# Kernel tuning notes

Hardware: AMD Instinct MI355X
Metric: run time of the kernel (lower is better)

Reference implementation:

```python
import jax, jax.numpy as jnp
import numpy as np

HEADS = 12
DIM_HEAD = 64

def setup_inputs() -> dict:
    key = jax.random.key(0)
    ks = jax.random.split(key, 5)
    B, S, D = 4, 2048, 768
    s = 0.02
    return {
        "x": jax.random.normal(ks[0], (B, S, D), dtype=jnp.float32),
        "Wq": jax.random.normal(ks[1], (D, D), dtype=jnp.float32) * s,
        "Wk": jax.random.normal(ks[2], (D, D), dtype=jnp.float32) * s,
        "Wv": jax.random.normal(ks[3], (D, D), dtype=jnp.float32) * s,
        "Wo": jax.random.normal(ks[4], (D, D), dtype=jnp.float32) * s,
        "bo": jnp.zeros((D,), dtype=jnp.float32),
    }

def reference(x, Wq, Wk, Wv, Wo, bo):
    B, S, D = x.shape
    H, Dh = HEADS, DIM_HEAD
    scale = Dh ** -0.5
    # projections (torch Linear: x @ W^T)
    q = (x @ Wq.T).reshape(B, S, H, Dh).transpose(0, 2, 1, 3) * scale  # [B,H,S,Dh]
    k = (x @ Wk.T).reshape(B, S, H, Dh).transpose(0, 2, 1, 3)
    v = (x @ Wv.T).reshape(B, S, H, Dh).transpose(0, 2, 1, 3)
    sim = jnp.einsum("bhid,bhjd->bhij", q, k)  # [B,H,S,S]
    mask_value = -jnp.finfo(sim.dtype).max
    causal_mask = jnp.triu(jnp.ones((S, S), dtype=bool), k=1)
    sim = jnp.where(causal_mask, mask_value, sim)
    attn = jax.nn.softmax(sim, axis=-1)
    # dropout is identity in eval mode
    out = jnp.einsum("bhij,bhjd->bhid", attn, v)  # [B,H,S,Dh]
    out = out.transpose(0, 2, 1, 3).reshape(B, S, H * Dh)
    return out @ Wo.T + bo
```

## Files before the change

### kernel.cpp

```cpp
#include <hip/hip_runtime.h>
#include <stdint.h>

typedef unsigned short u16;
typedef __bf16 bf16x8 __attribute__((ext_vector_type(8)));
typedef float f32x4 __attribute__((ext_vector_type(4)));
typedef u16 u16x4 __attribute__((ext_vector_type(4)));
typedef u16 u16x8 __attribute__((ext_vector_type(8)));
typedef uint32_t u32x2 __attribute__((ext_vector_type(2)));

#define LDS_CAST(p) (reinterpret_cast<__attribute__((address_space(3))) uint32_t*>(reinterpret_cast<uintptr_t>(p)))
#define GLB_CAST(p) (reinterpret_cast<const __attribute__((address_space(1))) uint32_t*>(reinterpret_cast<uintptr_t>(p)))
#define GLOAD16(g, l) __builtin_amdgcn_global_load_lds(GLB_CAST(g), LDS_CAST(l), 16, 0, 0)
#define AS3U16(p) (reinterpret_cast<__attribute__((address_space(3))) u16*>(reinterpret_cast<uintptr_t>(p)))

__device__ __forceinline__ u16 f2bf(float f) {
    uint32_t u = __builtin_bit_cast(uint32_t, f);
    u += 0x7fffu + ((u >> 16) & 1u);
    return (u16)(u >> 16);
}
__device__ __forceinline__ u16 bfbits(float f) {
    return __builtin_bit_cast(u16, (__bf16)f);
}

__global__ void cast_f32_bf16(const float* __restrict__ in, u16* __restrict__ out, int n4) {
    int i = blockIdx.x * blockDim.x + threadIdx.x;
    if (i >= n4) return;
    float4 f = reinterpret_cast<const float4*>(in)[i];
    u16x4 o;
    o.x = f2bf(f.x); o.y = f2bf(f.y); o.z = f2bf(f.z); o.w = f2bf(f.w);
    reinterpret_cast<u16x4*>(out)[i] = o;
}

__global__ void cast_w4(const float* __restrict__ a, const float* __restrict__ b,
                        const float* __restrict__ c, const float* __restrict__ d,
                        u16* __restrict__ oa, u16* __restrict__ ob,
                        u16* __restrict__ oc, u16* __restrict__ od, int n4) {
    const int z = blockIdx.y;
    const float* in = (z == 0) ? a : (z == 1) ? b : (z == 2) ? c : d;
    u16* out = (z == 0) ? oa : (z == 1) ? ob : (z == 2) ? oc : od;
    int i = blockIdx.x * blockDim.x + threadIdx.x;
    if (i >= n4) return;
    float4 f = reinterpret_cast<const float4*>(in)[i];
    u16x4 o;
    o.x = f2bf(f.x); o.y = f2bf(f.y); o.z = f2bf(f.z); o.w = f2bf(f.w);
    reinterpret_cast<u16x4*>(out)[i] = o;
}

__global__ __launch_bounds__(256) void gemm_qkv(
    const u16* __restrict__ X, const u16* __restrict__ Wq,
    const u16* __restrict__ Wk, const u16* __restrict__ Wv,
    u16* __restrict__ qo, u16* __restrict__ ko, u16* __restrict__ vTo)
{
    __shared__ u16 As[2][128 * 32];
    __shared__ u16 Bs[2][128 * 32];
    const int tid = threadIdx.x;
    const int lane = tid & 63;
    const int w = tid >> 6;
    const int lr = lane & 15, lg = lane >> 4;
    const int wrow = (w >> 1) * 64, wcol = (w & 1) * 64;

    const int lin = blockIdx.x + blockIdx.y * 6 + blockIdx.z * 384;
    const int xcd = lin & 7, idx = lin >> 3;
    const int prow = xcd * 8 + idx / 18;
    const int rem = idx % 18;
    const int bxc = rem % 6, z = rem / 6;
    const int row0 = prow * 128, col0 = bxc * 128;
    const u16* Wt = (z == 0) ? Wq : (z == 1) ? Wk : Wv;

    f32x4 acc[4][4];
#pragma unroll
    for (int m = 0; m < 4; ++m)
#pragma unroll
        for (int n = 0; n < 4; ++n)
#pragma unroll
            for (int j = 0; j < 4; ++j) acc[m][n][j] = 0.f;

#define QSTAGE(KT)                                                                                 \
    {                                                                                              \
        const int buf_ = (KT) & 1;                                                                 \
        _Pragma("unroll")                                                                          \
        for (int it = 0; it < 2; ++it) {                                                           \
            const int c = it * 256 + w * 64 + lane;                                                \
            const int row = c >> 2, c16 = c & 3;                                                   \
            GLOAD16(X  + (size_t)(row0 + row) * 768 + (KT) * 32 + c16 * 8, &As[buf_][(it * 256 + w * 64) * 8]); \
            GLOAD16(Wt + (size_t)(col0 + row) * 768 + (KT) * 32 + c16 * 8, &Bs[buf_][(it * 256 + w * 64) * 8]); \
        }                                                                                          \
    }

#define QSTEP(KT, VN, PF)                                                                          \
    {                                                                                              \
        if (PF) QSTAGE((KT) + 1);                                                                  \
        asm volatile("s_waitcnt vmcnt(" #VN ")" ::: "memory");                                     \
        __builtin_amdgcn_s_barrier();                                                              \
        const int cur_ = (KT) & 1;                                                                 \
        bf16x8 af[4], bfr[4];                                                                      \
        _Pragma("unroll")                                                                          \
        for (int m = 0; m < 4; ++m) af[m] = *(const bf16x8*)&As[cur_][(wrow + m * 16 + lr) * 32 + lg * 8]; \
        _Pragma("unroll")                                                                          \
        for (int n = 0; n < 4; ++n) bfr[n] = *(const bf16x8*)&Bs[cur_][(wcol + n * 16 + lr) * 32 + lg * 8]; \
        asm volatile("s_waitcnt lgkmcnt(0)" ::: "memory");                                         \
        __builtin_amdgcn_sched_barrier(0);                                                         \
        __builtin_amdgcn_s_barrier();                                                              \
        _Pragma("unroll")                                                                          \
        for (int m = 0; m < 4; ++m)                                                                \
            _Pragma("unroll")                                                                      \
            for (int n = 0; n < 4; ++n)                                                            \
                acc[m][n] = __builtin_amdgcn_mfma_f32_16x16x32_bf16(af[m], bfr[n], acc[m][n], 0, 0, 0); \
    }

    QSTAGE(0);
    for (int kt = 0; kt < 23; ++kt) QSTEP(kt, 4, true);
    QSTEP(23, 0, false);
#undef QSTEP
#undef QSTAGE

    if (z == 2) {
#pragma unroll
        for (int n = 0; n < 4; ++n) {
            const int j = col0 + wcol + n * 16 + lr;
            const int h = j >> 6, dh = j & 63;
#pragma unroll
            for (int m = 0; m < 4; ++m) {
                const int i0 = row0 + wrow + m * 16 + lg * 4;
                const int b = i0 >> 11, s0 = i0 & 2047;
                u16x4 pk;
#pragma unroll
                for (int r = 0; r < 4; ++r) pk[r] = bfbits(acc[m][n][r]);
                *(u16x4*)&vTo[(((size_t)b * 12 + h) * 64 + dh) * 2048 + s0] = pk;
            }
        }
    } else {
        u16* outp = (z == 0) ? qo : ko;
        const float scl = (z == 0) ? 0.18033688011112042f : 1.0f;
#pragma unroll
        for (int n = 0; n < 4; ++n) {
            const int j = col0 + wcol + n * 16 + lr;
            const int h = j >> 6, dh = j & 63;
#pragma unroll
            for (int m = 0; m < 4; ++m)
#pragma unroll
                for (int r = 0; r < 4; ++r) {
                    const int i = row0 + wrow + m * 16 + lg * 4 + r;
                    const int b = i >> 11, s = i & 2047;
                    outp[(((size_t)b * 12 + h) * 2048 + s) * 64 + dh] = bfbits(acc[m][n][r] * scl);
                }
        }
    }
}

template<bool DIAG>
__device__ __forceinline__ void attn_step(
    const bf16x8* aq, f32x4* o, float* lrow,
    const u16* __restrict__ Ksb, const u16* __restrict__ Vsb, u16* __restrict__ PT,
    int kvb, int qg0, int lr, int lg)
{
    f32x4 sacc[4];
#pragma unroll
    for (int n = 0; n < 4; ++n)
#pragma unroll
        for (int j = 0; j < 4; ++j) sacc[n][j] = 0.f;
    __builtin_amdgcn_s_setprio(1);
#pragma unroll
    for (int kk = 0; kk < 2; ++kk)
#pragma unroll
        for (int n = 0; n < 4; ++n) {
            const int row = n * 16 + lr;
            const int p = (kk * 4 + lg) ^ (row & 7);
            bf16x8 bk = *(const bf16x8*)&Ksb[row * 64 + p * 8];
            sacc[n] = __builtin_amdgcn_mfma_f32_16x16x32_bf16(aq[kk], bk, sacc[n], 0, 0, 0);
        }
    __builtin_amdgcn_s_setprio(0);

    float pv[4][4];
#pragma unroll
    for (int r = 0; r < 4; ++r) {
        float ls = 0.f;
#pragma unroll
        for (int n = 0; n < 4; ++n) {
            float sv = sacc[n][r];
            if (DIAG && (kvb + n * 16 + lr) > qg0 + r) sv = -1e30f;
            const float e = __builtin_amdgcn_exp2f(sv);
            pv[r][n] = e;
            ls += e;
        }
        lrow[r] += ls;
    }

#pragma unroll
    for (int n = 0; n < 4; ++n) {
        u16x4 pk;
#pragma unroll
        for (int r = 0; r < 4; ++r) pk[r] = bfbits(pv[r][n]);
        *(u16x4*)&PT[(n * 16 + lr) * 16 + lg * 4] = pk;
    }

    u32x2 t0, t1, t2, t3;
    __attribute__((address_space(3))) u16* pb = AS3U16(PT) + lg * 128 + lr * 4;
    asm volatile("ds_read_b64_tr_b16 %0, %1" : "=v"(t0) : "v"(pb) : "memory");
    asm volatile("ds_read_b64_tr_b16 %0, %1 offset:128" : "=v"(t1) : "v"(pb) : "memory");
    asm volatile("ds_read_b64_tr_b16 %0, %1 offset:1024" : "=v"(t2) : "v"(pb) : "memory");
    asm volatile("ds_read_b64_tr_b16 %0, %1 offset:1152" : "=v"(t3) : "v"(pb) : "memory");
    asm volatile("s_waitcnt lgkmcnt(0)" ::: "memory");
    __builtin_amdgcn_sched_barrier(0);
    union { u32x2 h[2]; bf16x8 v; } ua, ub;
    ua.h[0] = t0; ua.h[1] = t1;
    ub.h[0] = t2; ub.h[1] = t3;
    const bf16x8 ap0 = ua.v, ap1 = ub.v;

    __builtin_amdgcn_s_setprio(1);
#pragma unroll
    for (int n = 0; n < 4; ++n) {
        const int rowv = n * 16 + lr;
        const int p0 = (0 + lg) ^ (rowv & 7);
        const int p1 = (4 + lg) ^ (rowv & 7);
        bf16x8 bv0 = *(const bf16x8*)&Vsb[rowv * 64 + p0 * 8];
        bf16x8 bv1 = *(const bf16x8*)&Vsb[rowv * 64 + p1 * 8];
        o[n] = __builtin_amdgcn_mfma_f32_16x16x32_bf16(ap0, bv0, o[n], 0, 0, 0);
        o[n] = __builtin_amdgcn_mfma_f32_16x16x32_bf16(ap1, bv1, o[n], 0, 0, 0);
    }
    __builtin_amdgcn_s_setprio(0);
}

__global__ __launch_bounds__(256) void attn_kernel(
    const u16* __restrict__ q, const u16* __restrict__ k,
    const u16* __restrict__ vT, u16* __restrict__ attn)
{
    __shared__ u16 Ks[2][64 * 64];
    __shared__ u16 Vs[2][64 * 64];
    __shared__ u16 Ps[4][64 * 16];

    const int lin = blockIdx.x + (blockIdx.y << 4);
    const int logi = (lin & 7) * 96 + (lin >> 3);
    const int pair = logi & 15, bh = logi >> 4;

    const int qA = pair, qB = 31 - pair;
    const int tid = threadIdx.x, lane = tid & 63, w = tid >> 6;
    const int lr = lane & 15, lg = lane >> 4;

    const u16* Kp = k + (size_t)bh * 2048 * 64;
    const u16* Vp = vT + (size_t)bh * 64 * 2048;

    const u16* QpA = q + ((size_t)bh * 2048 + qA * 64 + w * 16) * 64;
    const u16* QpB = q + ((size_t)bh * 2048 + qB * 64 + w * 16) * 64;
    bf16x8 aqA[2], aqB[2];
    aqA[0] = *(const bf16x8*)&QpA[lr * 64 + lg * 8];
    aqA[1] = *(const bf16x8*)&QpA[lr * 64 + 32 + lg * 8];
    aqB[0] = *(const bf16x8*)&QpB[lr * 64 + lg * 8];
    aqB[1] = *(const bf16x8*)&QpB[lr * 64 + 32 + lg * 8];

    f32x4 oA[4], oB[4];
    float lA[4], lB[4];
#pragma unroll
    for (int n = 0; n < 4; ++n)
#pragma unroll
        for (int j = 0; j < 4; ++j) { oA[n][j] = 0.f; oB[n][j] = 0.f; }
#pragma unroll
    for (int r = 0; r < 4; ++r) { lA[r] = 0.f; lB[r] = 0.f; }

#define STAGE(T, BUF)                                                                        \
    {                                                                                        \
        _Pragma("unroll")                                                                    \
        for (int it = 0; it < 2; ++it) {                                                     \
            const int c = it * 256 + w * 64 + lane;                                          \
            const int row = c >> 3, pc = c & 7;                                              \
            const int lc = pc ^ (row & 7);                                                   \
            GLOAD16(Kp + (size_t)((T) * 64 + row) * 64 + lc * 8, &Ks[BUF][(it * 256 + w * 64) * 8]); \
            GLOAD16(Vp + (size_t)row * 2048 + (T) * 64 + lc * 8, &Vs[BUF][(it * 256 + w * 64) * 8]); \
        }                                                                                    \
    }

    STAGE(0, 0);
    const int qg0A = qA * 64 + w * 16 + lg * 4;
    const int qg0B = qB * 64 + w * 16 + lg * 4;

    int t = 0;
    for (; t < qA; ++t) {
        const int cur = t & 1;
        __syncthreads();
        STAGE(t + 1, cur ^ 1);
        attn_step<false>(aqB, oB, lB, Ks[cur], Vs[cur], Ps[w], t * 64, qg0B, lr, lg);
        attn_step<false>(aqA, oA, lA, Ks[cur], Vs[cur], Ps[w], t * 64, qg0A, lr, lg);
    }
    {
        const int cur = t & 1;
        __syncthreads();
        STAGE(t + 1, cur ^ 1);
        attn_step<false>(aqB, oB, lB, Ks[cur], Vs[cur], Ps[w], t * 64, qg0B, lr, lg);
        attn_step<true >(aqA, oA, lA, Ks[cur], Vs[cur], Ps[w], t * 64, qg0A, lr, lg);
        ++t;
    }
    for (; t < qB; ++t) {
        const int cur = t & 1;
        __syncthreads();
        STAGE(t + 1, cur ^ 1);
        attn_step<false>(aqB, oB, lB, Ks[cur], Vs[cur], Ps[w], t * 64, qg0B, lr, lg);
    }
    {
        const int cur = t & 1;
        __syncthreads();
        attn_step<true >(aqB, oB, lB, Ks[cur], Vs[cur], Ps[w], t * 64, qg0B, lr, lg);
    }
#undef STAGE

#pragma unroll
    for (int r = 0; r < 4; ++r) {
#pragma unroll
        for (int off = 1; off < 16; off <<= 1) {
            lA[r] += __shfl_xor(lA[r], off);
            lB[r] += __shfl_xor(lB[r], off);
        }
        lA[r] = 1.f / lA[r];
        lB[r] = 1.f / lB[r];
    }

    const int b = bh / 12, h = bh - b * 12;
#pragma unroll
    for (int n = 0; n < 4; ++n)
#pragma unroll
        for (int r = 0; r < 4; ++r) {
            const int sA = qA * 64 + w * 16 + lg * 4 + r;
            const int sB = qB * 64 + w * 16 + lg * 4 + r;
            attn[((size_t)b * 2048 + sA) * 768 + h * 64 + n * 16 + lr] = bfbits(oA[n][r] * lA[r]);
            attn[((size_t)b * 2048 + sB) * 768 + h * 64 + n * 16 + lr] = bfbits(oB[n][r] * lB[r]);
        }
}

__global__ __launch_bounds__(256) void gemm_out(
    const u16* __restrict__ A, const u16* __restrict__ Wo,
    const float* __restrict__ bo, float* __restrict__ out)
{
    __shared__ u16 As[2][128 * 32];
    __shared__ u16 Bs[2][128 * 32];
    const int tid = threadIdx.x;
    const int lane = tid & 63;
    const int w = tid >> 6;
    const int lr = lane & 15, lg = lane >> 4;
    const int wrow = (w >> 1) * 64, wcol = (w & 1) * 64;

    const int lin = blockIdx.x + blockIdx.y * 6;
    const int xcd = lin & 7, idx = lin >> 3;
    const int prow = xcd * 8 + idx / 6;
    const int bxc = idx % 6;
    const int row0 = prow * 128, col0 = bxc * 128;

    f32x4 acc[4][4];
#pragma unroll
    for (int m = 0; m < 4; ++m)
#pragma unroll
        for (int n = 0; n < 4; ++n)
#pragma unroll
            for (int j = 0; j < 4; ++j) acc[m][n][j] = 0.f;

#define OSTAGE(KT)                                                                                 \
    {                                                                                              \
        const int buf_ = (KT) & 1;                                                                 \
        _Pragma("unroll")                                                                          \
        for (int it = 0; it < 2; ++it) {                                                           \
            const int c = it * 256 + w * 64 + lane;                                                \
            const int row = c >> 2, c16 = c & 3;                                                   \
            GLOAD16(A  + (size_t)(row0 + row) * 768 + (KT) * 32 + c16 * 8, &As[buf_][(it * 256 + w * 64) * 8]); \
            GLOAD16(Wo + (size_t)(col0 + row) * 768 + (KT) * 32 + c16 * 8, &Bs[buf_][(it * 256 + w * 64) * 8]); \
        }                                                                                          \
    }

#define OSTEP(KT, VN, PF)                                                                          \
    {                                                                                              \
        if (PF) OSTAGE((KT) + 1);                                                                  \
        asm volatile("s_waitcnt vmcnt(" #VN ")" ::: "memory");                                     \
        __builtin_amdgcn_s_barrier();                                                              \
        const int cur_ = (KT) & 1;                                                                 \
        bf16x8 af[4], bfr[4];                                                                      \
        _Pragma("unroll")                                                                          \
        for (int m = 0; m < 4; ++m) af[m] = *(const bf16x8*)&As[cur_][(wrow + m * 16 + lr) * 32 + lg * 8]; \
        _Pragma("unroll")                                                                          \
        for (int n = 0; n < 4; ++n) bfr[n] = *(const bf16x8*)&Bs[cur_][(wcol + n * 16 + lr) * 32 + lg * 8]; \
        asm volatile("s_waitcnt lgkmcnt(0)" ::: "memory");                                         \
        __builtin_amdgcn_sched_barrier(0);                                                         \
        __builtin_amdgcn_s_barrier();                                                              \
        _Pragma("unroll")                                                                          \
        for (int m = 0; m < 4; ++m)                                                                \
            _Pragma("unroll")                                                                      \
            for (int n = 0; n < 4; ++n)                                                            \
                acc[m][n] = __builtin_amdgcn_mfma_f32_16x16x32_bf16(af[m], bfr[n], acc[m][n], 0, 0, 0); \
    }

    OSTAGE(0);
    for (int kt = 0; kt < 23; ++kt) OSTEP(kt, 4, true);
    OSTEP(23, 0, false);
#undef OSTEP
#undef OSTAGE

#pragma unroll
    for (int n = 0; n < 4; ++n) {
        const int j = col0 + wcol + n * 16 + lr;
        const float bj = bo[j];
#pragma unroll
        for (int m = 0; m < 4; ++m)
#pragma unroll
            for (int r = 0; r < 4; ++r) {
                const int i = row0 + wrow + m * 16 + lg * 4 + r;
                out[(size_t)i * 768 + j] = acc[m][n][r] + bj;
            }
    }
}

extern "C" void kernel_launch(void* const* d_in, const int* in_sizes, int n_in,
                              void* d_out, int out_size, void* d_ws, size_t ws_size,
                              hipStream_t stream) {
    const float* x  = (const float*)d_in[0];
    const float* Wq = (const float*)d_in[1];
    const float* Wk = (const float*)d_in[2];
    const float* Wv = (const float*)d_in[3];
    const float* Wo = (const float*)d_in[4];
    const float* bo = (const float*)d_in[5];
    float* out = (float*)d_out;

    const size_t NX = 6291456;
    const size_t NW = 589824;
    if (ws_size < (NX * 4 + NW * 4 + NX) * sizeof(u16)) return;
    u16* ws  = (u16*)d_ws;
    u16* xb  = ws;
    u16* wqb = xb  + NX;
    u16* wkb = wqb + NW;
    u16* wvb = wkb + NW;
    u16* wob = wvb + NW;
    u16* qb_ = wob + NW;
    u16* kb_ = qb_ + NX;
    u16* vtb = kb_ + NX;
    u16* ab_ = vtb + NX;

    cast_f32_bf16<<<6144, 256, 0, stream>>>(x, xb, (int)(NX / 4));
    cast_w4<<<dim3(576, 4), 256, 0, stream>>>(Wq, Wk, Wv, Wo, wqb, wkb, wvb, wob, (int)(NW / 4));

    gemm_qkv<<<dim3(6, 64, 3), 256, 0, stream>>>(xb, wqb, wkb, wvb, qb_, kb_, vtb);
    attn_kernel<<<dim3(16, 48), 256, 0, stream>>>(qb_, kb_, vtb, ab_);
    gemm_out<<<dim3(6, 64), 256, 0, stream>>>(ab_, wob, bo, out);
}
```

Baseline: 127.8 us.

## Merge cast kernels, share K/V fragments across query tiles, shrink output GEMM tile

Three separate changes. The two cast kernels become one launch, which removes a kernel launch. In attention, the K and V MFMA operand fragments are loaded from LDS once per KV tile into registers and reused by both query tiles (A and B), where before each attn_step reloaded them. The swizzle is also rewritten to use lr&7, which is equivalent to row&7 here. The output projection GEMM moves from 128x128 to 64x128 tiles with 768 blocks instead of 384, to fill more CUs, at the cost of more Wo traffic and higher register pressure from holding the fragments.

```diff
diff --git a/kernel.cpp b/kernel.cpp
--- a/kernel.cpp
+++ b/kernel.cpp
@@ -22,24 +22,24 @@
     return __builtin_bit_cast(u16, (__bf16)f);
 }
 
-__global__ void cast_f32_bf16(const float* __restrict__ in, u16* __restrict__ out, int n4) {
-    int i = blockIdx.x * blockDim.x + threadIdx.x;
-    if (i >= n4) return;
-    float4 f = reinterpret_cast<const float4*>(in)[i];
-    u16x4 o;
-    o.x = f2bf(f.x); o.y = f2bf(f.y); o.z = f2bf(f.z); o.w = f2bf(f.w);
-    reinterpret_cast<u16x4*>(out)[i] = o;
-}
-
-__global__ void cast_w4(const float* __restrict__ a, const float* __restrict__ b,
-                        const float* __restrict__ c, const float* __restrict__ d,
-                        u16* __restrict__ oa, u16* __restrict__ ob,
-                        u16* __restrict__ oc, u16* __restrict__ od, int n4) {
-    const int z = blockIdx.y;
-    const float* in = (z == 0) ? a : (z == 1) ? b : (z == 2) ? c : d;
-    u16* out = (z == 0) ? oa : (z == 1) ? ob : (z == 2) ? oc : od;
-    int i = blockIdx.x * blockDim.x + threadIdx.x;
-    if (i >= n4) return;
+__global__ void cast_all(const float* __restrict__ x,
+                         const float* __restrict__ a, const float* __restrict__ b,
+                         const float* __restrict__ c, const float* __restrict__ d,
+                         u16* __restrict__ ox, u16* __restrict__ oa, u16* __restrict__ ob,
+                         u16* __restrict__ oc, u16* __restrict__ od) {
+    const int bid = blockIdx.x;
+    const float* in;
+    u16* out;
+    int i;
+    if (bid < 6144) {
+        in = x; out = ox; i = bid * 256 + threadIdx.x;
+    } else {
+        const int zb = bid - 6144;
+        const int z = zb / 576, lb = zb % 576;
+        in = (z == 0) ? a : (z == 1) ? b : (z == 2) ? c : d;
+        out = (z == 0) ? oa : (z == 1) ? ob : (z == 2) ? oc : od;
+        i = lb * 256 + threadIdx.x;
+    }
     float4 f = reinterpret_cast<const float4*>(in)[i];
     u16x4 o;
     o.x = f2bf(f.x); o.y = f2bf(f.y); o.z = f2bf(f.z); o.w = f2bf(f.w);
@@ -148,10 +148,32 @@
     }
 }
 
+__device__ __forceinline__ void load_frags(
+    const u16* __restrict__ Ksb, const u16* __restrict__ Vsb,
+    bf16x8* bk, bf16x8* bv, int lr, int lg)
+{
+#pragma unroll
+    for (int kk = 0; kk < 2; ++kk)
+#pragma unroll
+        for (int n = 0; n < 4; ++n) {
+            const int row = n * 16 + lr;
+            const int p = (kk * 4 + lg) ^ (lr & 7);
+            bk[kk * 4 + n] = *(const bf16x8*)&Ksb[row * 64 + p * 8];
+        }
+#pragma unroll
+    for (int n = 0; n < 4; ++n) {
+        const int rowv = n * 16 + lr;
+        const int p0 = (0 + lg) ^ (lr & 7);
+        const int p1 = (4 + lg) ^ (lr & 7);
+        bv[n * 2 + 0] = *(const bf16x8*)&Vsb[rowv * 64 + p0 * 8];
+        bv[n * 2 + 1] = *(const bf16x8*)&Vsb[rowv * 64 + p1 * 8];
+    }
+}
+
 template<bool DIAG>
 __device__ __forceinline__ void attn_step(
-    const bf16x8* aq, f32x4* o, float* lrow,
-    const u16* __restrict__ Ksb, const u16* __restrict__ Vsb, u16* __restrict__ PT,
+    const bf16x8* aq, const bf16x8* bk, const bf16x8* bv,
+    f32x4* o, float* lrow, u16* __restrict__ PT,
     int kvb, int qg0, int lr, int lg)
 {
     f32x4 sacc[4];
@@ -163,12 +185,8 @@
 #pragma unroll
     for (int kk = 0; kk < 2; ++kk)
 #pragma unroll
-        for (int n = 0; n < 4; ++n) {
-            const int row = n * 16 + lr;
-            const int p = (kk * 4 + lg) ^ (row & 7);
-            bf16x8 bk = *(const bf16x8*)&Ksb[row * 64 + p * 8];
-            sacc[n] = __builtin_amdgcn_mfma_f32_16x16x32_bf16(aq[kk], bk, sacc[n], 0, 0, 0);
-        }
+        for (int n = 0; n < 4; ++n)
+            sacc[n] = __builtin_amdgcn_mfma_f32_16x16x32_bf16(aq[kk], bk[kk * 4 + n], sacc[n], 0, 0, 0);
     __builtin_amdgcn_s_setprio(0);
 
     float pv[4][4];
@@ -210,13 +228,8 @@
     __builtin_amdgcn_s_setprio(1);
 #pragma unroll
     for (int n = 0; n < 4; ++n) {
-        const int rowv = n * 16 + lr;
-        const int p0 = (0 + lg) ^ (rowv & 7);
-        const int p1 = (4 + lg) ^ (rowv & 7);
-        bf16x8 bv0 = *(const bf16x8*)&Vsb[rowv * 64 + p0 * 8];
-        bf16x8 bv1 = *(const bf16x8*)&Vsb[rowv * 64 + p1 * 8];
-        o[n] = __builtin_amdgcn_mfma_f32_16x16x32_bf16(ap0, bv0, o[n], 0, 0, 0);
-        o[n] = __builtin_amdgcn_mfma_f32_16x16x32_bf16(ap1, bv1, o[n], 0, 0, 0);
+        o[n] = __builtin_amdgcn_mfma_f32_16x16x32_bf16(ap0, bv[n * 2 + 0], o[n], 0, 0, 0);
+        o[n] = __builtin_amdgcn_mfma_f32_16x16x32_bf16(ap1, bv[n * 2 + 1], o[n], 0, 0, 0);
     }
     __builtin_amdgcn_s_setprio(0);
 }
@@ -273,32 +286,37 @@
     const int qg0A = qA * 64 + w * 16 + lg * 4;
     const int qg0B = qB * 64 + w * 16 + lg * 4;
 
+    bf16x8 bk[8], bv[8];
     int t = 0;
     for (; t < qA; ++t) {
         const int cur = t & 1;
         __syncthreads();
         STAGE(t + 1, cur ^ 1);
-        attn_step<false>(aqB, oB, lB, Ks[cur], Vs[cur], Ps[w], t * 64, qg0B, lr, lg);
-        attn_step<false>(aqA, oA, lA, Ks[cur], Vs[cur], Ps[w], t * 64, qg0A, lr, lg);
+        load_frags(Ks[cur], Vs[cur], bk, bv, lr, lg);
+        attn_step<false>(aqB, bk, bv, oB, lB, Ps[w], t * 64, qg0B, lr, lg);
+        attn_step<false>(aqA, bk, bv, oA, lA, Ps[w], t * 64, qg0A, lr, lg);
     }
     {
         const int cur = t & 1;
         __syncthreads();
         STAGE(t + 1, cur ^ 1);
-        attn_step<false>(aqB, oB, lB, Ks[cur], Vs[cur], Ps[w], t * 64, qg0B, lr, lg);
-        attn_step<true >(aqA, oA, lA, Ks[cur], Vs[cur], Ps[w], t * 64, qg0A, lr, lg);
+        load_frags(Ks[cur], Vs[cur], bk, bv, lr, lg);
+        attn_step<false>(aqB, bk, bv, oB, lB, Ps[w], t * 64, qg0B, lr, lg);
+        attn_step<true >(aqA, bk, bv, oA, lA, Ps[w], t * 64, qg0A, lr, lg);
         ++t;
     }
     for (; t < qB; ++t) {
         const int cur = t & 1;
         __syncthreads();
         STAGE(t + 1, cur ^ 1);
-        attn_step<false>(aqB, oB, lB, Ks[cur], Vs[cur], Ps[w], t * 64, qg0B, lr, lg);
+        load_frags(Ks[cur], Vs[cur], bk, bv, lr, lg);
+        attn_step<false>(aqB, bk, bv, oB, lB, Ps[w], t * 64, qg0B, lr, lg);
     }
     {
         const int cur = t & 1;
         __syncthreads();
-        attn_step<true >(aqB, oB, lB, Ks[cur], Vs[cur], Ps[w], t * 64, qg0B, lr, lg);
+        load_frags(Ks[cur], Vs[cur], bk, bv, lr, lg);
+        attn_step<true >(aqB, bk, bv, oB, lB, Ps[w], t * 64, qg0B, lr, lg);
     }
 #undef STAGE
 
@@ -329,23 +347,23 @@
     const u16* __restrict__ A, const u16* __restrict__ Wo,
     const float* __restrict__ bo, float* __restrict__ out)
 {
-    __shared__ u16 As[2][128 * 32];
+    __shared__ u16 As[2][64 * 32];
     __shared__ u16 Bs[2][128 * 32];
     const int tid = threadIdx.x;
     const int lane = tid & 63;
     const int w = tid >> 6;
     const int lr = lane & 15, lg = lane >> 4;
-    const int wrow = (w >> 1) * 64, wcol = (w & 1) * 64;
+    const int wrow = (w >> 1) * 32, wcol = (w & 1) * 64;
 
     const int lin = blockIdx.x + blockIdx.y * 6;
     const int xcd = lin & 7, idx = lin >> 3;
-    const int prow = xcd * 8 + idx / 6;
+    const int prow = xcd * 16 + idx / 6;
     const int bxc = idx % 6;
-    const int row0 = prow * 128, col0 = bxc * 128;
-
-    f32x4 acc[4][4];
-#pragma unroll
-    for (int m = 0; m < 4; ++m)
+    const int row0 = prow * 64, col0 = bxc * 128;
+
+    f32x4 acc[2][4];
+#pragma unroll
+    for (int m = 0; m < 2; ++m)
 #pragma unroll
         for (int n = 0; n < 4; ++n)
 #pragma unroll
@@ -354,12 +372,16 @@
 #define OSTAGE(KT)                                                                                 \
     {                                                                                              \
         const int buf_ = (KT) & 1;                                                                 \
-        _Pragma("unroll")                                                                          \
-        for (int it = 0; it < 2; ++it) {                                                           \
+        {                                                           \
+            const int c = w * 64 + lane;                                                           \
+            const int row = c >> 2, c16 = c & 3;                                                   \
+            GLOAD16(A + (size_t)(row0 + row) * 768 + (KT) * 32 + c16 * 8, &As[buf_][c * 8]);       \
+        }                                                                                          \
+        _Pragma("unroll")                                                                          \
+        for (int it = 0; it < 2; ++it) {                          \
             const int c = it * 256 + w * 64 + lane;                                                \
             const int row = c >> 2, c16 = c & 3;                                                   \
-            GLOAD16(A  + (size_t)(row0 + row) * 768 + (KT) * 32 + c16 * 8, &As[buf_][(it * 256 + w * 64) * 8]); \
-            GLOAD16(Wo + (size_t)(col0 + row) * 768 + (KT) * 32 + c16 * 8, &Bs[buf_][(it * 256 + w * 64) * 8]); \
+            GLOAD16(Wo + (size_t)(col0 + row) * 768 + (KT) * 32 + c16 * 8, &Bs[buf_][c * 8]);      \
         }                                                                                          \
     }
 
@@ -369,23 +391,23 @@
         asm volatile("s_waitcnt vmcnt(" #VN ")" ::: "memory");                                     \
         __builtin_amdgcn_s_barrier();                                                              \
         const int cur_ = (KT) & 1;                                                                 \
-        bf16x8 af[4], bfr[4];                                                                      \
-        _Pragma("unroll")                                                                          \
-        for (int m = 0; m < 4; ++m) af[m] = *(const bf16x8*)&As[cur_][(wrow + m * 16 + lr) * 32 + lg * 8]; \
+        bf16x8 af[2], bfr[4];                                                                      \
+        _Pragma("unroll")                                                                          \
+        for (int m = 0; m < 2; ++m) af[m] = *(const bf16x8*)&As[cur_][(wrow + m * 16 + lr) * 32 + lg * 8]; \
         _Pragma("unroll")                                                                          \
         for (int n = 0; n < 4; ++n) bfr[n] = *(const bf16x8*)&Bs[cur_][(wcol + n * 16 + lr) * 32 + lg * 8]; \
         asm volatile("s_waitcnt lgkmcnt(0)" ::: "memory");                                         \
         __builtin_amdgcn_sched_barrier(0);                                                         \
         __builtin_amdgcn_s_barrier();                                                              \
         _Pragma("unroll")                                                                          \
-        for (int m = 0; m < 4; ++m)                                                                \
+        for (int m = 0; m < 2; ++m)                                                                \
             _Pragma("unroll")                                                                      \
             for (int n = 0; n < 4; ++n)                                                            \
                 acc[m][n] = __builtin_amdgcn_mfma_f32_16x16x32_bf16(af[m], bfr[n], acc[m][n], 0, 0, 0); \
     }
 
     OSTAGE(0);
-    for (int kt = 0; kt < 23; ++kt) OSTEP(kt, 4, true);
+    for (int kt = 0; kt < 23; ++kt) OSTEP(kt, 3, true);
     OSTEP(23, 0, false);
 #undef OSTEP
 #undef OSTAGE
@@ -395,7 +417,7 @@
         const int j = col0 + wcol + n * 16 + lr;
         const float bj = bo[j];
 #pragma unroll
-        for (int m = 0; m < 4; ++m)
+        for (int m = 0; m < 2; ++m)
 #pragma unroll
             for (int r = 0; r < 4; ++r) {
                 const int i = row0 + wrow + m * 16 + lg * 4 + r;
@@ -429,10 +451,9 @@
     u16* vtb = kb_ + NX;
     u16* ab_ = vtb + NX;
 
-    cast_f32_bf16<<<6144, 256, 0, stream>>>(x, xb, (int)(NX / 4));
-    cast_w4<<<dim3(576, 4), 256, 0, stream>>>(Wq, Wk, Wv, Wo, wqb, wkb, wvb, wob, (int)(NW / 4));
+    cast_all<<<6144 + 2304, 256, 0, stream>>>(x, Wq, Wk, Wv, Wo, xb, wqb, wkb, wvb, wob);
 
     gemm_qkv<<<dim3(6, 64, 3), 256, 0, stream>>>(xb, wqb, wkb, wvb, qb_, kb_, vtb);
     attn_kernel<<<dim3(16, 48), 256, 0, stream>>>(qb_, kb_, vtb, ab_);
-    gemm_out<<<dim3(6, 64), 256, 0, stream>>>(ab_, wob, bo, out);
-}
+    gemm_out<<<dim3(6, 128), 256, 0, stream>>>(ab_, wob, bo, out);
+}
```

After: 136.9 us. +7.1%, slower.
